# Kernel tuning notes

Measured on AMD Instinct MI355X. Metric: run time of the kernel, lower is better.

The kernel has to match this reference:

```python
import jax, jax.numpy as jnp
import numpy as np

NUM_USERS = 200000
NUM_ARTISTS = 50000
LATENT_DIM = 64
NUM_EDGES = 2000000
NUM_LAYERS = 3


def setup_inputs() -> dict:
    key = jax.random.key(0)
    k_u, k_a, k_src, k_dst = jax.random.split(key, 4)
    x_users = jax.random.normal(k_u, (NUM_USERS, LATENT_DIM), dtype=jnp.float32)
    x_artists = jax.random.normal(k_a, (NUM_ARTISTS, LATENT_DIM), dtype=jnp.float32)
    # a2u: row 0 = artist (source) ids, row 1 = user (target) ids
    art = jax.random.randint(k_src, (NUM_EDGES,), 0, NUM_ARTISTS, dtype=jnp.int32)
    usr = jax.random.randint(k_dst, (NUM_EDGES,), 0, NUM_USERS, dtype=jnp.int32)
    edge_index_a2u = jnp.stack([art, usr], axis=0)
    # u2a is the reversed edge list: row 0 = user (source), row 1 = artist (target)
    edge_index_u2a = jnp.stack([usr, art], axis=0)
    return {
        "x_users": x_users,
        "x_artists": x_artists,
        "edge_index_a2u": edge_index_a2u,
        "edge_index_u2a": edge_index_u2a,
    }


def _scatter_mean(src_nodes, edge_index, dim_size):
    """Gather src_nodes[edge_index[0]] and scatter-mean onto edge_index[1].

    Matches torch_scatter.scatter(reduce='mean'): empty segments yield 0.
    """
    msgs = src_nodes[edge_index[0]]                     # [E, D] gather
    sums = jax.ops.segment_sum(msgs, edge_index[1], num_segments=dim_size)
    ones = jnp.ones((edge_index.shape[1],), dtype=src_nodes.dtype)
    counts = jax.ops.segment_sum(ones, edge_index[1], num_segments=dim_size)
    return sums / jnp.maximum(counts, 1.0)[:, None]


def reference(x_users, x_artists, edge_index_a2u, edge_index_u2a):
    scale = 1.0 / (NUM_LAYERS + 1)
    final_u = x_users * scale
    final_a = x_artists * scale
    for _ in range(NUM_LAYERS):
        x_users = _scatter_mean(x_artists, edge_index_a2u, NUM_USERS)
        x_artists = _scatter_mean(x_users, edge_index_u2a, NUM_ARTISTS)
        final_u = final_u + x_users * scale
        final_a = final_a + x_artists * scale
    return final_u, final_a
```

## Files before the change

kernel.cpp:

```cpp
#include <hip/hip_runtime.h>
#include <hip/hip_fp16.h>

#define D 64
#define TB 256

#define BSHIFT_U 10
#define BSHIFT_A 8
#define CAP 12288

typedef _Float16 half8 __attribute__((ext_vector_type(8)));
typedef float float8 __attribute__((ext_vector_type(8)));

__device__ __forceinline__ float8 h8_to_f8(half8 h) {
    return __builtin_convertvector(h, float8);
}

__global__ __launch_bounds__(TB) void zero_ints_kernel(int* __restrict__ p, int n) {
    int i = blockIdx.x * blockDim.x + threadIdx.x;
    int stride = gridDim.x * blockDim.x;
    for (; i < n; i += stride) p[i] = 0;
}

__global__ __launch_bounds__(TB) void cvt_f16_kernel(const float4* __restrict__ in,
                                                     half8* __restrict__ out, int n8) {
    int i = blockIdx.x * blockDim.x + threadIdx.x;
    int stride = gridDim.x * blockDim.x;
    for (; i < n8; i += stride) {
        float4 a = in[i * 2 + 0];
        float4 b = in[i * 2 + 1];
        half8 h;
        h[0] = (_Float16)a.x; h[1] = (_Float16)a.y; h[2] = (_Float16)a.z; h[3] = (_Float16)a.w;
        h[4] = (_Float16)b.x; h[5] = (_Float16)b.y; h[6] = (_Float16)b.z; h[7] = (_Float16)b.w;
        out[i] = h;
    }
}

__global__ __launch_bounds__(TB) void partition_both_kernel(const int* __restrict__ art,
                                                            const int* __restrict__ usr, int E,
                                                            int* __restrict__ bcur_u,
                                                            int* __restrict__ bcur_a,
                                                            unsigned* __restrict__ part_u,
                                                            unsigned* __restrict__ part_a,
                                                            int NBu, int NBa) {
    __shared__ int cu[256], bu[256], ca[256], ba[256];
    for (int i = threadIdx.x; i < NBu; i += TB) cu[i] = 0;
    for (int i = threadIdx.x; i < NBa; i += TB) ca[i] = 0;
    __syncthreads();
    int chunk = (E + gridDim.x - 1) / gridDim.x;
    int e0 = blockIdx.x * chunk;
    int e1 = min(E, e0 + chunk);
    for (int e = e0 + threadIdx.x; e < e1; e += TB) {
        atomicAdd(&cu[usr[e] >> BSHIFT_U], 1);
        atomicAdd(&ca[art[e] >> BSHIFT_A], 1);
    }
    __syncthreads();
    for (int i = threadIdx.x; i < NBu; i += TB) {
        int c = cu[i];
        bu[i] = c ? (i * CAP + atomicAdd(&bcur_u[i], c)) : 0;
        cu[i] = 0;
    }
    for (int i = threadIdx.x; i < NBa; i += TB) {
        int c = ca[i];
        ba[i] = c ? (i * CAP + atomicAdd(&bcur_a[i], c)) : 0;
        ca[i] = 0;
    }
    __syncthreads();
    for (int e = e0 + threadIdx.x; e < e1; e += TB) {
        int a = art[e];
        int u = usr[e];
        int bui = u >> BSHIFT_U;
        int lu = atomicAdd(&cu[bui], 1);
        part_u[bu[bui] + lu] = ((unsigned)a << BSHIFT_U) | ((unsigned)u & ((1u << BSHIFT_U) - 1u));
        int bai = a >> BSHIFT_A;
        int la = atomicAdd(&ca[bai], 1);
        part_a[ba[bai] + la] = ((unsigned)u << BSHIFT_A) | ((unsigned)a & ((1u << BSHIFT_A) - 1u));
    }
}

__device__ __forceinline__ void local_csr_body(const unsigned* __restrict__ part,
                                               int ecount, int ebeg, int n0,
                                               int* __restrict__ row_beg,
                                               int* __restrict__ deg_arr,
                                               int* __restrict__ csr,
                                               int N, int NPB, int BSHIFT,
                                               int* cnt, int* sdata) {
    const int tid = threadIdx.x;
    const int eend = ebeg + ecount;
    const unsigned mask = (unsigned)(NPB - 1);
    for (int i = tid; i < NPB; i += TB) cnt[i] = 0;
    __syncthreads();
    for (int e = ebeg + tid; e < eend; e += TB)
        atomicAdd(&cnt[part[e] & mask], 1);
    __syncthreads();
    const int ITEMS = NPB >> 8;
    const int ib = tid * ITEMS;
    int local = 0;
    for (int k = 0; k < ITEMS; ++k) local += cnt[ib + k];
    sdata[tid] = local;
    __syncthreads();
    for (int off = 1; off < TB; off <<= 1) {
        int t = (tid >= off) ? sdata[tid - off] : 0;
        __syncthreads();
        if (tid >= off) sdata[tid] += t;
        __syncthreads();
    }
    int run = sdata[tid] - local;
    for (int k = 0; k < ITEMS; ++k) {
        int v = cnt[ib + k];
        cnt[ib + k] = run;
        int n = n0 + ib + k;
        if (n < N) { row_beg[n] = ebeg + run; deg_arr[n] = v; }
        run += v;
    }
    __syncthreads();
    for (int e = ebeg + tid; e < eend; e += TB) {
        unsigned r = part[e];
        int l = (int)(r & mask);
        int pos = atomicAdd(&cnt[l], 1);
        csr[ebeg + pos] = (int)(r >> BSHIFT);
    }
}

__global__ __launch_bounds__(TB) void local_csr_both_kernel(const unsigned* __restrict__ part_u,
                                                            const unsigned* __restrict__ part_a,
                                                            const int* __restrict__ bcur_u,
                                                            const int* __restrict__ bcur_a,
                                                            int* __restrict__ row_beg_u,
                                                            int* __restrict__ deg_u,
                                                            int* __restrict__ row_beg_a,
                                                            int* __restrict__ deg_a,
                                                            int* __restrict__ csr_u,
                                                            int* __restrict__ csr_a,
                                                            int NU, int NA, int NBu) {
    __shared__ int cnt[1024];
    __shared__ int sdata[TB];
    const int b = blockIdx.x;
    if (b < NBu) {
        local_csr_body(part_u, bcur_u[b], b * CAP, b << BSHIFT_U,
                       row_beg_u, deg_u, csr_u, NU, 1 << BSHIFT_U, BSHIFT_U, cnt, sdata);
    } else {
        const int bb = b - NBu;
        local_csr_body(part_a, bcur_a[bb], bb * CAP, bb << BSHIFT_A,
                       row_beg_a, deg_a, csr_a, NA, 1 << BSHIFT_A, BSHIFT_A, cnt, sdata);
    }
}

__global__ __launch_bounds__(TB) void gather_mean_kernel(const half8* __restrict__ src,
                                                         const int* __restrict__ csr,
                                                         const int* __restrict__ row_beg,
                                                         const int* __restrict__ deg_arr,
                                                         half8* __restrict__ x_out,
                                                         float4* __restrict__ final_acc,
                                                         const float4* __restrict__ init_src,
                                                         int N, float scale) {
    const int lane = threadIdx.x & 7;
    int g = (blockIdx.x * blockDim.x + threadIdx.x) >> 3;
    const int ngroups = (gridDim.x * blockDim.x) >> 3;
    for (int n = g; n < N; n += ngroups) {
        const int beg = row_beg[n];
        const int dg = deg_arr[n];
        const int end = beg + dg;
        float8 a0 = 0.f, a1 = 0.f, a2 = 0.f, a3 = 0.f;
        int e = beg;
        for (; e + 4 <= end; e += 4) {
            const int s0 = csr[e + 0];
            const int s1 = csr[e + 1];
            const int s2 = csr[e + 2];
            const int s3 = csr[e + 3];
            const half8 v0 = src[s0 * 8 + lane];
            const half8 v1 = src[s1 * 8 + lane];
            const half8 v2 = src[s2 * 8 + lane];
            const half8 v3 = src[s3 * 8 + lane];
            a0 += h8_to_f8(v0);
            a1 += h8_to_f8(v1);
            a2 += h8_to_f8(v2);
            a3 += h8_to_f8(v3);
        }
        for (; e < end; ++e)
            a0 += h8_to_f8(src[csr[e] * 8 + lane]);
        float8 s = (a0 + a1) + (a2 + a3);
        const float inv = 1.f / (float)(dg > 0 ? dg : 1);
        float8 x = s * inv;
        half8 h;
        for (int k = 0; k < 8; ++k) h[k] = (_Float16)x[k];
        x_out[n * 8 + lane] = h;
        if (final_acc != nullptr) {
            const int fo = n * (D / 4) + lane * 2;
            float4 f0, f1;
            if (init_src != nullptr) {
                f0 = init_src[fo + 0];
                f1 = init_src[fo + 1];
                f0.x *= scale; f0.y *= scale; f0.z *= scale; f0.w *= scale;
                f1.x *= scale; f1.y *= scale; f1.z *= scale; f1.w *= scale;
            } else {
                f0 = final_acc[fo + 0];
                f1 = final_acc[fo + 1];
            }
            f0.x += x[0] * scale; f0.y += x[1] * scale; f0.z += x[2] * scale; f0.w += x[3] * scale;
            f1.x += x[4] * scale; f1.y += x[5] * scale; f1.z += x[6] * scale; f1.w += x[7] * scale;
            final_acc[fo + 0] = f0;
            final_acc[fo + 1] = f1;
        }
    }
}

__global__ __launch_bounds__(TB) void final_sum_kernel(const float4* __restrict__ in0,
                                                       const half8* __restrict__ x1,
                                                       const half8* __restrict__ x2,
                                                       const half8* __restrict__ x3,
                                                       float4* __restrict__ out,
                                                       int n8, float scale) {
    int i = blockIdx.x * blockDim.x + threadIdx.x;
    int stride = gridDim.x * blockDim.x;
    for (; i < n8; i += stride) {
        float8 s = h8_to_f8(x1[i]) + h8_to_f8(x2[i]) + h8_to_f8(x3[i]);
        float4 a = in0[i * 2 + 0];
        float4 b = in0[i * 2 + 1];
        a.x = (a.x + s[0]) * scale; a.y = (a.y + s[1]) * scale;
        a.z = (a.z + s[2]) * scale; a.w = (a.w + s[3]) * scale;
        b.x = (b.x + s[4]) * scale; b.y = (b.y + s[5]) * scale;
        b.z = (b.z + s[6]) * scale; b.w = (b.w + s[7]) * scale;
        out[i * 2 + 0] = a;
        out[i * 2 + 1] = b;
    }
}

extern "C" void kernel_launch(void* const* d_in, const int* in_sizes, int n_in,
                              void* d_out, int out_size, void* d_ws, size_t ws_size,
                              hipStream_t stream) {
    const float* x_users   = (const float*)d_in[0];
    const float* x_artists = (const float*)d_in[1];
    const int*   a2u       = (const int*)d_in[2];

    const int NU = in_sizes[0] / D;
    const int NA = in_sizes[1] / D;
    const int E  = in_sizes[2] / 2;
    const int* art = a2u;
    const int* usr = a2u + E;

    const float scale = 0.25f;

    const int NBu = (NU + (1 << BSHIFT_U) - 1) >> BSHIFT_U;
    const int NBa = (NA + (1 << BSHIFT_A) - 1) >> BSHIFT_A;

    char* w = (char*)d_ws;
    size_t off = 0;
    auto alloc = [&](size_t bytes) -> char* {
        char* p = w + off;
        off += (bytes + 255) & ~(size_t)255;
        return p;
    };
    int* row_beg_u = (int*)alloc((size_t)NU * 4);
    int* deg_u     = (int*)alloc((size_t)NU * 4);
    int* row_beg_a = (int*)alloc((size_t)NA * 4);
    int* deg_a     = (int*)alloc((size_t)NA * 4);
    int* bcur      = (int*)alloc((size_t)(NBu + NBa) * 4);
    int* bcur_u    = bcur;
    int* bcur_a    = bcur + NBu;
    int* csr_u     = (int*)alloc((size_t)NBu * CAP * 4);
    int* csr_a     = (int*)alloc((size_t)NBa * CAP * 4);
    half8* xa_in   = (half8*)alloc((size_t)NA * D * 2);
    unsigned* part_u = (unsigned*)alloc((size_t)NBu * CAP * 4);
    unsigned* part_a = (unsigned*)alloc((size_t)NBa * CAP * 4);

    const size_t XU = (size_t)NU * D * 2;
    const size_t XA = (size_t)NA * D * 2;
    const size_t XUa = (XU + 255) & ~(size_t)255;
    const size_t XAa = (XA + 255) & ~(size_t)255;

    const bool modeA = (off + 3 * XUa) <= ws_size;

    half8* x_u1 = (half8*)alloc(XU);
    half8* x_u2 = modeA ? (half8*)alloc(XU) : x_u1;
    half8* x_u3 = modeA ? (half8*)alloc(XU) : x_u1;
    char* part_base = (char*)part_u;
    half8* x_a1 = (half8*)(part_base);
    half8* x_a2 = modeA ? (half8*)(part_base + XAa) : x_a1;
    half8* x_a3 = modeA ? (half8*)(part_base + 2 * XAa) : x_a1;

    float* out_u = (float*)d_out;
    float* out_a = out_u + (size_t)NU * D;

    cvt_f16_kernel<<<1024, TB, 0, stream>>>((const float4*)x_artists, xa_in, NA * D / 8);
    zero_ints_kernel<<<1, TB, 0, stream>>>(bcur, NBu + NBa);
    partition_both_kernel<<<512, TB, 0, stream>>>(art, usr, E, bcur_u, bcur_a,
                                                  part_u, part_a, NBu, NBa);
    local_csr_both_kernel<<<NBu + NBa, TB, 0, stream>>>(part_u, part_a, bcur_u, bcur_a,
                                                        row_beg_u, deg_u, row_beg_a, deg_a,
                                                        csr_u, csr_a, NU, NA, NBu);

    half8* xu_buf[3] = {x_u1, x_u2, x_u3};
    half8* xa_buf[3] = {x_a1, x_a2, x_a3};
    const half8* srcA = xa_in;
    for (int l = 0; l < 3; ++l) {
        gather_mean_kernel<<<4096, TB, 0, stream>>>(
            srcA, csr_u, row_beg_u, deg_u, xu_buf[l],
            modeA ? nullptr : (float4*)out_u,
            (!modeA && l == 0) ? (const float4*)x_users : nullptr, NU, scale);
        gather_mean_kernel<<<4096, TB, 0, stream>>>(
            xu_buf[l], csr_a, row_beg_a, deg_a, xa_buf[l],
            modeA ? nullptr : (float4*)out_a,
            (!modeA && l == 0) ? (const float4*)x_artists : nullptr, NA, scale);
        srcA = xa_buf[l];
    }

    if (modeA) {
        final_sum_kernel<<<4096, TB, 0, stream>>>((const float4*)x_users,
                                                  x_u1, x_u2, x_u3,
                                                  (float4*)out_u, NU * D / 8, scale);
        final_sum_kernel<<<2048, TB, 0, stream>>>((const float4*)x_artists,
                                                  x_a1, x_a2, x_a3,
                                                  (float4*)out_a, NA * D / 8, scale);
    }
}
```

Before: 388.2 us.

## Fuse final sum into last gather, pack row/degree, XCD-partition edge binning

After: 477.0 us. 1.23x slower.

```diff
diff --git a/kernel.cpp b/kernel.cpp
--- a/kernel.cpp
+++ b/kernel.cpp
@@ -7,6 +7,7 @@
 #define BSHIFT_U 10
 #define BSHIFT_A 8
 #define CAP 12288
+#define NXCD 8
 
 typedef _Float16 half8 __attribute__((ext_vector_type(8)));
 typedef float float8 __attribute__((ext_vector_type(8)));
@@ -43,15 +44,20 @@
                                                             unsigned* __restrict__ part_a,
                                                             int NBu, int NBa) {
     __shared__ int cu[256], bu[256], ca[256], ba[256];
+    const int g   = blockIdx.x & (NXCD - 1);
+    const int sub = blockIdx.x >> 3;
+    const int nsub = gridDim.x >> 3;
     for (int i = threadIdx.x; i < NBu; i += TB) cu[i] = 0;
     for (int i = threadIdx.x; i < NBa; i += TB) ca[i] = 0;
     __syncthreads();
-    int chunk = (E + gridDim.x - 1) / gridDim.x;
-    int e0 = blockIdx.x * chunk;
+    int chunk = (E + nsub - 1) / nsub;
+    int e0 = sub * chunk;
     int e1 = min(E, e0 + chunk);
     for (int e = e0 + threadIdx.x; e < e1; e += TB) {
-        atomicAdd(&cu[usr[e] >> BSHIFT_U], 1);
-        atomicAdd(&ca[art[e] >> BSHIFT_A], 1);
+        int bui = usr[e] >> BSHIFT_U;
+        if ((bui & (NXCD - 1)) == g) atomicAdd(&cu[bui], 1);
+        int bai = art[e] >> BSHIFT_A;
+        if (((bai + NBu) & (NXCD - 1)) == g) atomicAdd(&ca[bai], 1);
     }
     __syncthreads();
     for (int i = threadIdx.x; i < NBu; i += TB) {
@@ -69,18 +75,21 @@
         int a = art[e];
         int u = usr[e];
         int bui = u >> BSHIFT_U;
-        int lu = atomicAdd(&cu[bui], 1);
-        part_u[bu[bui] + lu] = ((unsigned)a << BSHIFT_U) | ((unsigned)u & ((1u << BSHIFT_U) - 1u));
+        if ((bui & (NXCD - 1)) == g) {
+            int lu = atomicAdd(&cu[bui], 1);
+            part_u[bu[bui] + lu] = ((unsigned)a << BSHIFT_U) | ((unsigned)u & ((1u << BSHIFT_U) - 1u));
+        }
         int bai = a >> BSHIFT_A;
-        int la = atomicAdd(&ca[bai], 1);
-        part_a[ba[bai] + la] = ((unsigned)u << BSHIFT_A) | ((unsigned)a & ((1u << BSHIFT_A) - 1u));
+        if (((bai + NBu) & (NXCD - 1)) == g) {
+            int la = atomicAdd(&ca[bai], 1);
+            part_a[ba[bai] + la] = ((unsigned)u << BSHIFT_A) | ((unsigned)a & ((1u << BSHIFT_A) - 1u));
+        }
     }
 }
 
 __device__ __forceinline__ void local_csr_body(const unsigned* __restrict__ part,
                                                int ecount, int ebeg, int n0,
-                                               int* __restrict__ row_beg,
-                                               int* __restrict__ deg_arr,
+                                               int2* __restrict__ rowdeg,
                                                int* __restrict__ csr,
                                                int N, int NPB, int BSHIFT,
                                                int* cnt, int* sdata) {
@@ -109,7 +118,7 @@
         int v = cnt[ib + k];
         cnt[ib + k] = run;
         int n = n0 + ib + k;
-        if (n < N) { row_beg[n] = ebeg + run; deg_arr[n] = v; }
+        if (n < N) rowdeg[n] = make_int2(ebeg + run, v);
         run += v;
     }
     __syncthreads();
@@ -125,10 +134,8 @@
                                                             const unsigned* __restrict__ part_a,
                                                             const int* __restrict__ bcur_u,
                                                             const int* __restrict__ bcur_a,
-                                                            int* __restrict__ row_beg_u,
-                                                            int* __restrict__ deg_u,
-                                                            int* __restrict__ row_beg_a,
-                                                            int* __restrict__ deg_a,
+                                                            int2* __restrict__ rowdeg_u,
+                                                            int2* __restrict__ rowdeg_a,
                                                             int* __restrict__ csr_u,
                                                             int* __restrict__ csr_a,
                                                             int NU, int NA, int NBu) {
@@ -137,28 +144,32 @@
     const int b = blockIdx.x;
     if (b < NBu) {
         local_csr_body(part_u, bcur_u[b], b * CAP, b << BSHIFT_U,
-                       row_beg_u, deg_u, csr_u, NU, 1 << BSHIFT_U, BSHIFT_U, cnt, sdata);
+                       rowdeg_u, csr_u, NU, 1 << BSHIFT_U, BSHIFT_U, cnt, sdata);
     } else {
         const int bb = b - NBu;
         local_csr_body(part_a, bcur_a[bb], bb * CAP, bb << BSHIFT_A,
-                       row_beg_a, deg_a, csr_a, NA, 1 << BSHIFT_A, BSHIFT_A, cnt, sdata);
+                       rowdeg_a, csr_a, NA, 1 << BSHIFT_A, BSHIFT_A, cnt, sdata);
     }
 }
 
 __global__ __launch_bounds__(TB) void gather_mean_kernel(const half8* __restrict__ src,
                                                          const int* __restrict__ csr,
-                                                         const int* __restrict__ row_beg,
-                                                         const int* __restrict__ deg_arr,
+                                                         const int2* __restrict__ rowdeg,
                                                          half8* __restrict__ x_out,
                                                          float4* __restrict__ final_acc,
                                                          const float4* __restrict__ init_src,
+                                                         const float4* __restrict__ fin_in0,
+                                                         const half8* __restrict__ fin_x1,
+                                                         const half8* __restrict__ fin_x2,
+                                                         float4* __restrict__ fin_out,
                                                          int N, float scale) {
     const int lane = threadIdx.x & 7;
     int g = (blockIdx.x * blockDim.x + threadIdx.x) >> 3;
     const int ngroups = (gridDim.x * blockDim.x) >> 3;
     for (int n = g; n < N; n += ngroups) {
-        const int beg = row_beg[n];
-        const int dg = deg_arr[n];
+        const int2 rd = rowdeg[n];
+        const int beg = rd.x;
+        const int dg = rd.y;
         const int end = beg + dg;
         float8 a0 = 0.f, a1 = 0.f, a2 = 0.f, a3 = 0.f;
         int e = beg;
@@ -181,11 +192,25 @@
         float8 s = (a0 + a1) + (a2 + a3);
         const float inv = 1.f / (float)(dg > 0 ? dg : 1);
         float8 x = s * inv;
-        half8 h;
-        for (int k = 0; k < 8; ++k) h[k] = (_Float16)x[k];
-        x_out[n * 8 + lane] = h;
+        const int o8 = n * 8 + lane;
+        if (x_out != nullptr) {
+            half8 h;
+            for (int k = 0; k < 8; ++k) h[k] = (_Float16)x[k];
+            x_out[o8] = h;
+        }
+        const int fo = n * (D / 4) + lane * 2;
+        if (fin_out != nullptr) {
+            float8 t = h8_to_f8(fin_x1[o8]) + h8_to_f8(fin_x2[o8]) + x;
+            float4 f0 = fin_in0[fo + 0];
+            float4 f1 = fin_in0[fo + 1];
+            f0.x = (f0.x + t[0]) * scale; f0.y = (f0.y + t[1]) * scale;
+            f0.z = (f0.z + t[2]) * scale; f0.w = (f0.w + t[3]) * scale;
+            f1.x = (f1.x + t[4]) * scale; f1.y = (f1.y + t[5]) * scale;
+            f1.z = (f1.z + t[6]) * scale; f1.w = (f1.w + t[7]) * scale;
+            fin_out[fo + 0] = f0;
+            fin_out[fo + 1] = f1;
+        }
         if (final_acc != nullptr) {
-            const int fo = n * (D / 4) + lane * 2;
             float4 f0, f1;
             if (init_src != nullptr) {
                 f0 = init_src[fo + 0];
@@ -204,27 +229,6 @@
     }
 }
 
-__global__ __launch_bounds__(TB) void final_sum_kernel(const float4* __restrict__ in0,
-                                                       const half8* __restrict__ x1,
-                                                       const half8* __restrict__ x2,
-                                                       const half8* __restrict__ x3,
-                                                       float4* __restrict__ out,
-                                                       int n8, float scale) {
-    int i = blockIdx.x * blockDim.x + threadIdx.x;
-    int stride = gridDim.x * blockDim.x;
-    for (; i < n8; i += stride) {
-        float8 s = h8_to_f8(x1[i]) + h8_to_f8(x2[i]) + h8_to_f8(x3[i]);
-        float4 a = in0[i * 2 + 0];
-        float4 b = in0[i * 2 + 1];
-        a.x = (a.x + s[0]) * scale; a.y = (a.y + s[1]) * scale;
-        a.z = (a.z + s[2]) * scale; a.w = (a.w + s[3]) * scale;
-        b.x = (b.x + s[4]) * scale; b.y = (b.y + s[5]) * scale;
-        b.z = (b.z + s[6]) * scale; b.w = (b.w + s[7]) * scale;
-        out[i * 2 + 0] = a;
-        out[i * 2 + 1] = b;
-    }
-}
-
 extern "C" void kernel_launch(void* const* d_in, const int* in_sizes, int n_in,
                               void* d_out, int out_size, void* d_ws, size_t ws_size,
                               hipStream_t stream) {
@@ -250,10 +254,8 @@
         off += (bytes + 255) & ~(size_t)255;
         return p;
     };
-    int* row_beg_u = (int*)alloc((size_t)NU * 4);
-    int* deg_u     = (int*)alloc((size_t)NU * 4);
-    int* row_beg_a = (int*)alloc((size_t)NA * 4);
-    int* deg_a     = (int*)alloc((size_t)NA * 4);
+    int2* rowdeg_u = (int2*)alloc((size_t)NU * 8);
+    int2* rowdeg_a = (int2*)alloc((size_t)NA * 8);
     int* bcur      = (int*)alloc((size_t)(NBu + NBa) * 4);
     int* bcur_u    = bcur;
     int* bcur_a    = bcur + NBu;
@@ -286,30 +288,33 @@
     partition_both_kernel<<<512, TB, 0, stream>>>(art, usr, E, bcur_u, bcur_a,
                                                   part_u, part_a, NBu, NBa);
     local_csr_both_kernel<<<NBu + NBa, TB, 0, stream>>>(part_u, part_a, bcur_u, bcur_a,
-                                                        row_beg_u, deg_u, row_beg_a, deg_a,
+                                                        rowdeg_u, rowdeg_a,
                                                         csr_u, csr_a, NU, NA, NBu);
 
     half8* xu_buf[3] = {x_u1, x_u2, x_u3};
     half8* xa_buf[3] = {x_a1, x_a2, x_a3};
     const half8* srcA = xa_in;
     for (int l = 0; l < 3; ++l) {
+        const bool last = (l == 2);
         gather_mean_kernel<<<4096, TB, 0, stream>>>(
-            srcA, csr_u, row_beg_u, deg_u, xu_buf[l],
+            srcA, csr_u, rowdeg_u, xu_buf[l],
             modeA ? nullptr : (float4*)out_u,
-            (!modeA && l == 0) ? (const float4*)x_users : nullptr, NU, scale);
+            (!modeA && l == 0) ? (const float4*)x_users : nullptr,
+            (modeA && last) ? (const float4*)x_users : nullptr,
+            (modeA && last) ? x_u1 : nullptr,
+            (modeA && last) ? x_u2 : nullptr,
+            (modeA && last) ? (float4*)out_u : nullptr,
+            NU, scale);
         gather_mean_kernel<<<4096, TB, 0, stream>>>(
-            xu_buf[l], csr_a, row_beg_a, deg_a, xa_buf[l],
+            xu_buf[l], csr_a, rowdeg_a,
+            (modeA && last) ? nullptr : xa_buf[l],
             modeA ? nullptr : (float4*)out_a,
-            (!modeA && l == 0) ? (const float4*)x_artists : nullptr, NA, scale);
+            (!modeA && l == 0) ? (const float4*)x_artists : nullptr,
+            (modeA && last) ? (const float4*)x_artists : nullptr,
+            (modeA && last) ? x_a1 : nullptr,
+            (modeA && last) ? x_a2 : nullptr,
+            (modeA && last) ? (float4*)out_a : nullptr,
+            NA, scale);
         srcA = xa_buf[l];
     }
-
-    if (modeA) {
-        final_sum_kernel<<<4096, TB, 0, stream>>>((const float4*)x_users,
-                                                  x_u1, x_u2, x_u3,
-                                                  (float4*)out_u, NU * D / 8, scale);
-        final_sum_kernel<<<2048, TB, 0, stream>>>((const float4*)x_artists,
-                                                  x_a1, x_a2, x_a3,
-                                                  (float4*)out_a, NA * D / 8, scale);
-    }
-}
+}
```
